# Performance work log

Hardware: AMD Instinct MI355X
Metric: run time of the kernel (lower is better)

Reference implementation:

```python
import jax, jax.numpy as jnp
import numpy as np

MAX_LENGTH = 252
HID = 768
MLP = 770
NLAB = 36


def setup_inputs() -> dict:
    key = jax.random.key(0)
    ks = jax.random.split(key, 7)
    B = 2
    hidden = jax.random.normal(ks[0], (B, MAX_LENGTH + 1, HID), dtype=jnp.float32)
    pred_spans = jnp.sort(jax.random.randint(ks[1], (B, 2), 0, MAX_LENGTH), axis=1)
    span_mask = jax.random.randint(ks[2], (MAX_LENGTH, MAX_LENGTH), 0, 2).astype(jnp.int32)
    W1 = jax.random.normal(ks[3], (MLP, 2 * HID + 1), dtype=jnp.float32) * 0.02
    b1 = jax.random.normal(ks[4], (MLP,), dtype=jnp.float32) * 0.02
    W2 = jax.random.normal(ks[5], (NLAB, MLP), dtype=jnp.float32) * 0.02
    b2 = jax.random.normal(ks[6], (NLAB,), dtype=jnp.float32) * 0.02
    return {"hidden": hidden, "pred_spans": pred_spans, "span_mask": span_mask,
            "W1": W1, "b1": b1, "W2": W2, "b2": b2}


def reference(hidden, pred_spans, span_mask, W1, b1, W2, b2):
    L = MAX_LENGTH
    B = hidden.shape[0]
    vecs = hidden[:, 1:L + 1, :]                      # [B, L, 768] (skip [CLS])
    # Split concat-weight: feat = [vec_i, vec_j, indicator]
    W1i = W1[:, :HID]                                 # [770, 768]
    W1j = W1[:, HID:2 * HID]                          # [770, 768]
    w1c = W1[:, 2 * HID]                              # [770]
    Ai = jnp.einsum('bld,hd->blh', vecs, W1i)         # [B, L, 770]
    Aj = jnp.einsum('bld,hd->blh', vecs, W1j)         # [B, L, 770]
    # Predicate-span indicator: 2 if (i,j)==pred_span; 1 if strictly inside
    # combinations_with_replacement(start..end) minus (start,end); else 0.
    ii = jnp.arange(L)[:, None]
    jj = jnp.arange(L)[None, :]
    s = pred_spans[:, 0][:, None, None]
    e = pred_spans[:, 1][:, None, None]
    eq = (ii == s) & (jj == e)
    inside = (s <= ii) & (ii <= jj) & (jj <= e)
    ind = jnp.where(eq, 2.0, jnp.where(inside, 1.0, 0.0)).astype(hidden.dtype)  # [B,L,L]
    h = Ai[:, :, None, :] + Aj[:, None, :, :] + ind[..., None] * w1c + b1       # [B,L,L,770]
    h = jax.nn.relu(h)
    out = jnp.einsum('bijh,kh->bijk', h, W2) + b2     # [B, L, L, 36]
    valid = (span_mask >= 1)[None, :, :, None]
    out = jnp.where(valid, out, 0.0)                  # invalid pairs -> exact zeros
    out = out.reshape(B, L * L, NLAB)                 # pair dim = 63504
    res = jax.nn.log_softmax(out, axis=1)             # softmax over span pairs
    return jnp.transpose(res, (0, 2, 1))              # [B, 36, L*L]
```

## Files before the change

kernel.cpp:

```cpp
#include <hip/hip_runtime.h>
#include <hip/hip_bf16.h>
#include <math.h>

#define L 252
#define HID 768
#define MLP 770
#define NLAB 36
#define NB 2
#define M1 (NB*L)
#define N1 (2*MLP)
#define LL (L*L)
#define LL4 (LL/4)
#define KC 25
#define KC1 24

typedef float f32x4 __attribute__((ext_vector_type(4)));
typedef short short8 __attribute__((ext_vector_type(8)));

#define AJF_OFF 0
#define AJF_FLOATS 204800
#define AIB_OFF (AJF_OFF + AJF_FLOATS)
#define AIB_FLOATS 604800
#define W2F_OFF (AIB_OFF + AIB_FLOATS)
#define W2F_FLOATS 19200
#define PART_OFF (W2F_OFF + W2F_FLOATS)
#define PART_FLOATS (72*1024*2)

__device__ __forceinline__ void dma16(const void* g, void* l) {
  __builtin_amdgcn_global_load_lds(
      (const __attribute__((address_space(1))) unsigned int*)g,
      (__attribute__((address_space(3))) unsigned int*)l, 16, 0, 0);
}

__device__ __forceinline__ unsigned short bf16b(float x) {
  __hip_bfloat16 h = __float2bfloat16(x);
  return *reinterpret_cast<unsigned short*>(&h);
}

__global__ __launch_bounds__(256) void gemm1_kernel(const float* __restrict__ hid,
                                                    const float* __restrict__ b1,
                                                    const float* __restrict__ W1,
                                                    const float* __restrict__ W2,
                                                    unsigned short* __restrict__ AJF,
                                                    unsigned short* __restrict__ AiBh,
                                                    uint4* __restrict__ W2F) {
  int t = threadIdx.x;
  if (blockIdx.y == 0 && t < 192) {
    int kcw = blockIdx.x;
    int tile = t / 64, lane2 = t - tile * 64;
    int label = tile * 16 + (lane2 & 15);
    int kb = kcw * 32 + (lane2 >> 4) * 8;
    unsigned int u[4];
#pragma unroll
    for (int p = 0; p < 4; p++) {
      unsigned short us[2];
#pragma unroll
      for (int q = 0; q < 2; q++) {
        int k = kb + 2 * p + q;
        float v = (label < NLAB && k < MLP) ? W2[label * MLP + k] : 0.f;
        us[q] = bf16b(v);
      }
      u[p] = (unsigned int)us[0] | ((unsigned int)us[1] << 16);
    }
    W2F[kcw * 192 + t] = make_uint4(u[0], u[1], u[2], u[3]);
  }

  int wave = t >> 6, lane = t & 63, lj = lane & 15, kh = lane >> 4;
  int nt0 = blockIdx.x * 4;
  int m0 = blockIdx.y * 64 + wave * 16;
  int m = m0 + lj;
  int mc = (m < M1) ? m : (M1 - 1);
  int bb = (mc >= L) ? 1 : 0;
  const float* hrow = hid + ((size_t)(bb * (L + 1) + 1 + (mc - bb * L))) * HID + kh * 8;

  const float* rp[4];
#pragma unroll
  for (int nt = 0; nt < 4; nt++) {
    int n = (nt0 + nt) * 16 + lj;
    int nc = (n < N1) ? n : 0;
    rp[nt] = (nc < MLP) ? (W1 + (size_t)nc * 1537)
                        : (W1 + (size_t)(nc - MLP) * 1537 + HID);
  }

  f32x4 acc[4];
#pragma unroll
  for (int nt = 0; nt < 4; nt++) acc[nt] = (f32x4)(0.f);

  union FU { unsigned u[4]; short8 s8; };

  float4 h0 = *(const float4*)(hrow);
  float4 h1 = *(const float4*)(hrow + 4);
  float bw[4][8];
#pragma unroll
  for (int nt = 0; nt < 4; nt++)
#pragma unroll
    for (int e = 0; e < 8; e++) bw[nt][e] = rp[nt][kh * 8 + e];

  for (int kc = 0; kc < KC1; kc++) {
    FU af;
    {
      __hip_bfloat162 p0 = __float22bfloat162_rn(make_float2(h0.x, h0.y));
      __hip_bfloat162 p1 = __float22bfloat162_rn(make_float2(h0.z, h0.w));
      __hip_bfloat162 p2 = __float22bfloat162_rn(make_float2(h1.x, h1.y));
      __hip_bfloat162 p3 = __float22bfloat162_rn(make_float2(h1.z, h1.w));
      af.u[0] = *reinterpret_cast<unsigned*>(&p0);
      af.u[1] = *reinterpret_cast<unsigned*>(&p1);
      af.u[2] = *reinterpret_cast<unsigned*>(&p2);
      af.u[3] = *reinterpret_cast<unsigned*>(&p3);
    }
    FU cb[4];
#pragma unroll
    for (int nt = 0; nt < 4; nt++) {
#pragma unroll
      for (int q = 0; q < 4; q++) {
        __hip_bfloat162 pk = __float22bfloat162_rn(make_float2(bw[nt][2 * q], bw[nt][2 * q + 1]));
        cb[nt].u[q] = *reinterpret_cast<unsigned*>(&pk);
      }
    }
    int kn = kc + 1;
    if (kn < KC1) {
      h0 = *(const float4*)(hrow + kn * 32);
      h1 = *(const float4*)(hrow + kn * 32 + 4);
#pragma unroll
      for (int nt = 0; nt < 4; nt++)
#pragma unroll
        for (int e = 0; e < 8; e++) bw[nt][e] = rp[nt][kn * 32 + kh * 8 + e];
    }
#pragma unroll
    for (int nt = 0; nt < 4; nt++)
      acc[nt] = __builtin_amdgcn_mfma_f32_16x16x32_bf16(af.s8, cb[nt].s8, acc[nt], 0, 0, 0);
  }

#pragma unroll
  for (int nt = 0; nt < 4; nt++) {
    int nn = (nt0 + nt) * 16 + lj;
    if (nn >= N1) continue;
    if (nn < MLP) {
      float b1v = b1[nn];
      float wv = W1[(size_t)nn * 1537 + 1536];
#pragma unroll
      for (int r = 0; r < 4; r++) {
        int mm = m0 + kh * 4 + r;
        if (mm < M1) {
          float a = acc[nt][r] + b1v;
          AiBh[(size_t)(0 * M1 + mm) * 800 + nn] = bf16b(a);
          AiBh[(size_t)(1 * M1 + mm) * 800 + nn] = bf16b(a + wv);
          AiBh[(size_t)(2 * M1 + mm) * 800 + nn] = bf16b(a + 2.f * wv);
        }
      }
    } else {
      int hh = nn - MLP;
      int kcq = hh >> 5, kk = hh & 31;
      int l2hi = (kk >> 3) << 4, ee = kk & 7;
#pragma unroll
      for (int r = 0; r < 4; r++) {
        int mm = m0 + kh * 4 + r;
        if (mm < M1) {
          int bb2 = (mm >= L) ? 1 : 0;
          int jg = mm - bb2 * L;
          size_t rec = ((size_t)((bb2 * KC + kcq) * 16 + (jg >> 4)) * 64 + (l2hi | (jg & 15)));
          AJF[rec * 8 + ee] = bf16b(acc[nt][r]);
        }
      }
    }
  }
}

__global__ __launch_bounds__(256, 2) void main_kernel(
    const unsigned short* __restrict__ AJF,
    const unsigned short* __restrict__ AiBh,
    const uint4* __restrict__ wfr,
    const float* __restrict__ b2,
    const int* __restrict__ spans,
    const int* __restrict__ smask,
    float* __restrict__ out,
    float* __restrict__ part) {
  __shared__ char sm[16384];
  int t = threadIdx.x;
  int wave = t >> 6, lane = t & 63, lj = lane & 15, kh = lane >> 4;
  int j0 = blockIdx.x * 64;
  int i0 = blockIdx.y * 4;
  int b = blockIdx.z;
  int s = spans[2 * b], e = spans[2 * b + 1];
  int j = j0 + wave * 16 + lj;

  int pidx[4];
#pragma unroll
  for (int ii = 0; ii < 4; ii++) {
    int i = i0 + ii;
    int ind = 0;
    if (i == s && j == e) ind = 2;
    else if (s <= i && i <= j && j <= e) ind = 1;
    pidx[ii] = 256 + (ind * 4 + ii) * 4 + kh;
  }

  const unsigned short* aj_g = AJF + ((size_t)((b * KC + 0) * 16 + (j0 >> 4) + wave) * 64 + lane) * 8;
  int pr = lane >> 2; if (pr > 11) pr = 11;
  int pt = pr >> 2, pii = pr & 3, pc = lane & 3;
  const unsigned short* p_g = AiBh + (size_t)(pt * M1 + b * L + i0 + pii) * 800 + pc * 8;
  const uint4* wf_g = wfr + lane;

  f32x4 acc[4][3];
#pragma unroll
  for (int ii = 0; ii < 4; ii++)
#pragma unroll
    for (int tl = 0; tl < 3; tl++) acc[ii][tl] = (f32x4)(0.f);

  union FU { unsigned u[4]; short8 s8; };

  {
    char* bfb = sm;
    dma16(aj_g, bfb + (wave << 10));
    if (wave == 1) dma16(p_g, bfb + 4096);
    if (wave == 0) {
      dma16(&wf_g[0 * 64], bfb + 5120);
      dma16(&wf_g[1 * 64], bfb + 6144);
      dma16(&wf_g[2 * 64], bfb + 7168);
    }
  }

  for (int kc = 0; kc < KC; kc++) {
    __syncthreads();
    int kn = kc + 1;
    if (kn < KC) {
      char* bfb = sm + ((kn & 1) << 13);
      dma16(aj_g + (size_t)kn * 8192, bfb + (wave << 10));
      if (wave == 1) dma16(p_g + kn * 32, bfb + 4096);
      if (wave == 0) {
        dma16(&wf_g[(kn * 3 + 0) * 64], bfb + 5120);
        dma16(&wf_g[(kn * 3 + 1) * 64], bfb + 6144);
        dma16(&wf_g[(kn * 3 + 2) * 64], bfb + 7168);
      }
    }
    const uint4* bu = (const uint4*)(sm + ((kc & 1) << 13));
    uint4 av = bu[(wave << 6) + lane];
    uint4 w0 = bu[320 + lane];
    uint4 w1 = bu[384 + lane];
    uint4 w2v = bu[448 + lane];
    float ajf[8];
    ajf[0] = __uint_as_float(av.x << 16); ajf[1] = __uint_as_float(av.x & 0xFFFF0000u);
    ajf[2] = __uint_as_float(av.y << 16); ajf[3] = __uint_as_float(av.y & 0xFFFF0000u);
    ajf[4] = __uint_as_float(av.z << 16); ajf[5] = __uint_as_float(av.z & 0xFFFF0000u);
    ajf[6] = __uint_as_float(av.w << 16); ajf[7] = __uint_as_float(av.w & 0xFFFF0000u);
    FU wf0, wf1, wf2;
    wf0.u[0] = w0.x; wf0.u[1] = w0.y; wf0.u[2] = w0.z; wf0.u[3] = w0.w;
    wf1.u[0] = w1.x; wf1.u[1] = w1.y; wf1.u[2] = w1.z; wf1.u[3] = w1.w;
    wf2.u[0] = w2v.x; wf2.u[1] = w2v.y; wf2.u[2] = w2v.z; wf2.u[3] = w2v.w;
#pragma unroll
    for (int ii = 0; ii < 4; ii++) {
      uint4 pv = bu[pidx[ii]];
      unsigned pu[4] = {pv.x, pv.y, pv.z, pv.w};
      FU fr;
#pragma unroll
      for (int q = 0; q < 4; q++) {
        float x0 = fmaxf(ajf[2 * q] + __uint_as_float(pu[q] << 16), 0.f);
        float x1 = fmaxf(ajf[2 * q + 1] + __uint_as_float(pu[q] & 0xFFFF0000u), 0.f);
        __hip_bfloat162 pk = __float22bfloat162_rn(make_float2(x0, x1));
        fr.u[q] = *reinterpret_cast<unsigned*>(&pk);
      }
      acc[ii][0] = __builtin_amdgcn_mfma_f32_16x16x32_bf16(fr.s8, wf0.s8, acc[ii][0], 0, 0, 0);
      acc[ii][1] = __builtin_amdgcn_mfma_f32_16x16x32_bf16(fr.s8, wf1.s8, acc[ii][1], 0, 0, 0);
      acc[ii][2] = __builtin_amdgcn_mfma_f32_16x16x32_bf16(fr.s8, wf2.s8, acc[ii][2], 0, 0, 0);
    }
  }

  float v[4][3][4];
#pragma unroll
  for (int ii = 0; ii < 4; ii++) {
    int i = i0 + ii;
    int smv[4];
#pragma unroll
    for (int r = 0; r < 4; r++) {
      int jr = j0 + wave * 16 + kh * 4 + r;
      smv[r] = (jr < L) ? smask[(size_t)i * L + jr] : 0;
    }
#pragma unroll
    for (int tl = 0; tl < 3; tl++) {
      int label = tl * 16 + lj;
      bool lab_ok = label < NLAB;
      float bbv = lab_ok ? b2[label] : 0.f;
#pragma unroll
      for (int r = 0; r < 4; r++) {
        int jr = j0 + wave * 16 + kh * 4 + r;
        float vv = -1e30f;
        if (jr < L && lab_ok) {
          vv = (smv[r] >= 1) ? acc[ii][tl][r] + bbv : 0.f;
          out[(size_t)(b * NLAB + label) * LL + (size_t)i * L + jr] = vv;
        }
        v[ii][tl][r] = vv;
      }
    }
  }
#pragma unroll
  for (int tl = 0; tl < 3; tl++) {
    float mx = -1e30f;
#pragma unroll
    for (int ii = 0; ii < 4; ii++)
#pragma unroll
      for (int r = 0; r < 4; r++) mx = fmaxf(mx, v[ii][tl][r]);
    mx = fmaxf(mx, __shfl_xor(mx, 16, 64));
    mx = fmaxf(mx, __shfl_xor(mx, 32, 64));
    float ssum = 0.f;
#pragma unroll
    for (int ii = 0; ii < 4; ii++)
#pragma unroll
      for (int r = 0; r < 4; r++) {
        float vv = v[ii][tl][r];
        ssum += (vv > -1e29f) ? __expf(vv - mx) : 0.f;
      }
    ssum += __shfl_xor(ssum, 16, 64);
    ssum += __shfl_xor(ssum, 32, 64);
    int label = tl * 16 + lj;
    if (kh == 0 && label < NLAB) {
      int slot = (blockIdx.x * 63 + blockIdx.y) * 4 + wave;
      float2* pp = (float2*)part + (size_t)(b * NLAB + label) * 1024 + slot;
      *pp = make_float2(mx, ssum);
    }
  }
}

__global__ __launch_bounds__(256) void finish_kernel(const float* __restrict__ part,
                                                     float* __restrict__ out) {
  int bk = blockIdx.y, cx = blockIdx.x;
  int t = threadIdx.x, wave = t >> 6, lane = t & 63;
  const float2* pp = (const float2*)part + (size_t)bk * 1024;
  float m = -1e30f, ss = 0.f;
  for (int idx = t; idx < 1008; idx += 256) {
    float2 q = pp[idx];
    if (q.x > m) { ss = ss * __expf(m - q.x) + q.y; m = q.x; }
    else ss += q.y * __expf(q.x - m);
  }
#pragma unroll
  for (int o = 1; o < 64; o <<= 1) {
    float m2 = __shfl_xor(m, o, 64);
    float s2 = __shfl_xor(ss, o, 64);
    if (m2 > m) { ss = ss * __expf(m - m2) + s2; m = m2; }
    else ss += s2 * __expf(m2 - m);
  }
  __shared__ float rm[4], rs[4], lsh;
  if (lane == 0) { rm[wave] = m; rs[wave] = ss; }
  __syncthreads();
  if (t == 0) {
    float M = rm[0], S = rs[0];
#pragma unroll
    for (int w = 1; w < 4; w++) {
      float m2 = rm[w], s2 = rs[w];
      if (m2 > M) { S = S * __expf(M - m2) + s2; M = m2; }
      else S += s2 * __expf(m2 - M);
    }
    lsh = M + logf(S);
  }
  __syncthreads();
  float l = lsh;
  float4* po = (float4*)(out + (size_t)bk * LL);
  int start = cx * 1985;
  int end = start + 1985; if (end > LL4) end = LL4;
  for (int idx = start + t; idx < end; idx += 256) {
    float4 v = po[idx];
    v.x -= l; v.y -= l; v.z -= l; v.w -= l;
    po[idx] = v;
  }
}

extern "C" void kernel_launch(void* const* d_in, const int* in_sizes, int n_in,
                              void* d_out, int out_size, void* d_ws, size_t ws_size,
                              hipStream_t stream) {
  const float* hidden = (const float*)d_in[0];
  const int* spans    = (const int*)d_in[1];
  const int* smask    = (const int*)d_in[2];
  const float* W1     = (const float*)d_in[3];
  const float* b1     = (const float*)d_in[4];
  const float* W2     = (const float*)d_in[5];
  const float* b2     = (const float*)d_in[6];
  float* ws = (float*)d_ws;
  unsigned short* AJF  = (unsigned short*)(ws + AJF_OFF);
  unsigned short* AiBh = (unsigned short*)(ws + AIB_OFF);
  uint4* W2F           = (uint4*)(ws + W2F_OFF);
  float* part          = ws + PART_OFF;
  float* out = (float*)d_out;

  gemm1_kernel<<<dim3(25, 8), 256, 0, stream>>>(hidden, b1, W1, W2, AJF, AiBh, W2F);
  main_kernel<<<dim3(4, 63, NB), 256, 0, stream>>>(AJF, AiBh, (const uint4*)W2F, b2,
                                                   spans, smask, out, part);
  finish_kernel<<<dim3(8, NB * NLAB), 256, 0, stream>>>(part, out);
}
```

Before: 155.8 us.

## Prepack bf16 operands and use per-wave LDS DMA pipelines without block barriers

Adds a pack kernel that converts W1, W2 and the hidden rows to bf16 MFMA fragment layout ahead of time. gemm1 then streams these fragments through per-wave double-buffered LDS via global_load_lds instead of doing strided fp32 loads and converting inline. main_kernel drops __syncthreads: each wave loads its own copy of the P and W2 fragments into a private LDS region and waits only on its own vmcnt. This costs an extra launch, redundant per-wave loads, and more LDS per block (40 KB), which may lower occupancy.

```diff
diff --git a/kernel.cpp b/kernel.cpp
--- a/kernel.cpp
+++ b/kernel.cpp
@@ -13,6 +13,8 @@
 #define LL4 (LL/4)
 #define KC 25
 #define KC1 24
+#define NT1P 100
+#define NMT 32
 
 typedef float f32x4 __attribute__((ext_vector_type(4)));
 typedef short short8 __attribute__((ext_vector_type(8)));
@@ -25,6 +27,13 @@
 #define W2F_FLOATS 19200
 #define PART_OFF (W2F_OFF + W2F_FLOATS)
 #define PART_FLOATS (72*1024*2)
+#define W1F_OFF (PART_OFF + PART_FLOATS)
+#define W1F_FLOATS (KC1*NT1P*64*4)
+#define VBF_OFF (W1F_OFF + W1F_FLOATS)
+#define VBF_FLOATS (NMT*KC1*64*4)
+#define NW1F (KC1*NT1P*64)
+#define NW2F (KC*3*64)
+#define NVBF (NMT*KC1*64)
 
 __device__ __forceinline__ void dma16(const void* g, void* l) {
   __builtin_amdgcn_global_load_lds(
@@ -37,19 +46,42 @@
   return *reinterpret_cast<unsigned short*>(&h);
 }
 
-__global__ __launch_bounds__(256) void gemm1_kernel(const float* __restrict__ hid,
-                                                    const float* __restrict__ b1,
-                                                    const float* __restrict__ W1,
-                                                    const float* __restrict__ W2,
-                                                    unsigned short* __restrict__ AJF,
-                                                    unsigned short* __restrict__ AiBh,
-                                                    uint4* __restrict__ W2F) {
-  int t = threadIdx.x;
-  if (blockIdx.y == 0 && t < 192) {
-    int kcw = blockIdx.x;
-    int tile = t / 64, lane2 = t - tile * 64;
-    int label = tile * 16 + (lane2 & 15);
-    int kb = kcw * 32 + (lane2 >> 4) * 8;
+#define WAIT_VM0() __builtin_amdgcn_s_waitcnt(0x0F70)
+
+__global__ __launch_bounds__(256) void pack_kernel(const float* __restrict__ W1,
+                                                   const float* __restrict__ W2,
+                                                   const float* __restrict__ hid,
+                                                   float* __restrict__ ws) {
+  const int total = NW1F + NW2F + NVBF;
+  int idx = blockIdx.x * 256 + threadIdx.x;
+  if (idx >= total) return;
+  if (idx < NW1F) {
+    int kc = idx / (NT1P * 64);
+    int rem = idx - kc * (NT1P * 64);
+    int nt = rem / 64, lane = rem - nt * 64;
+    int n = nt * 16 + (lane & 15);
+    int kb = kc * 32 + (lane >> 4) * 8;
+    unsigned int u[4];
+#pragma unroll
+    for (int p = 0; p < 4; p++) {
+      unsigned short us[2];
+#pragma unroll
+      for (int q = 0; q < 2; q++) {
+        int k = kb + 2 * p + q;
+        float v = 0.f;
+        if (n < N1) v = (n < MLP) ? W1[(size_t)n * 1537 + k]
+                                  : W1[(size_t)(n - MLP) * 1537 + HID + k];
+        us[q] = bf16b(v);
+      }
+      u[p] = (unsigned int)us[0] | ((unsigned int)us[1] << 16);
+    }
+    ((uint4*)(ws + W1F_OFF))[idx] = make_uint4(u[0], u[1], u[2], u[3]);
+  } else if (idx < NW1F + NW2F) {
+    int e2 = idx - NW1F;
+    int kc = e2 / 192, rem = e2 - kc * 192;
+    int tile = rem / 64, lane = rem - tile * 64;
+    int label = tile * 16 + (lane & 15);
+    int kb = kc * 32 + (lane >> 4) * 8;
     unsigned int u[4];
 #pragma unroll
     for (int p = 0; p < 4; p++) {
@@ -62,73 +94,77 @@
       }
       u[p] = (unsigned int)us[0] | ((unsigned int)us[1] << 16);
     }
-    W2F[kcw * 192 + t] = make_uint4(u[0], u[1], u[2], u[3]);
-  }
-
+    ((uint4*)(ws + W2F_OFF))[e2] = make_uint4(u[0], u[1], u[2], u[3]);
+  } else {
+    int e3 = idx - NW1F - NW2F;
+    int mt = e3 / (KC1 * 64);
+    int rem = e3 - mt * (KC1 * 64);
+    int kc = rem / 64, lane = rem - kc * 64;
+    int m = mt * 16 + (lane & 15);
+    int kb = kc * 32 + (lane >> 4) * 8;
+    unsigned int u[4] = {0u, 0u, 0u, 0u};
+    if (m < M1) {
+      int b = (m >= L) ? 1 : 0;
+      const float* src = hid + ((size_t)(b * (L + 1) + 1 + (m - b * L))) * HID + kb;
+      float4 v0 = *(const float4*)src;
+      float4 v1 = *(const float4*)(src + 4);
+      float vv[8] = {v0.x, v0.y, v0.z, v0.w, v1.x, v1.y, v1.z, v1.w};
+#pragma unroll
+      for (int p = 0; p < 4; p++)
+        u[p] = (unsigned int)bf16b(vv[2 * p]) | ((unsigned int)bf16b(vv[2 * p + 1]) << 16);
+    }
+    ((uint4*)(ws + VBF_OFF))[e3] = make_uint4(u[0], u[1], u[2], u[3]);
+  }
+}
+
+__global__ __launch_bounds__(256, 2) void gemm1_kernel(const float* __restrict__ b1,
+                                                       const float* __restrict__ W1,
+                                                       const float* __restrict__ ws_ro,
+                                                       unsigned short* __restrict__ AJF,
+                                                       unsigned short* __restrict__ AiBh) {
+  __shared__ char sm[40960];
+  int t = threadIdx.x;
   int wave = t >> 6, lane = t & 63, lj = lane & 15, kh = lane >> 4;
   int nt0 = blockIdx.x * 4;
-  int m0 = blockIdx.y * 64 + wave * 16;
-  int m = m0 + lj;
-  int mc = (m < M1) ? m : (M1 - 1);
-  int bb = (mc >= L) ? 1 : 0;
-  const float* hrow = hid + ((size_t)(bb * (L + 1) + 1 + (mc - bb * L))) * HID + kh * 8;
-
-  const float* rp[4];
-#pragma unroll
-  for (int nt = 0; nt < 4; nt++) {
-    int n = (nt0 + nt) * 16 + lj;
-    int nc = (n < N1) ? n : 0;
-    rp[nt] = (nc < MLP) ? (W1 + (size_t)nc * 1537)
-                        : (W1 + (size_t)(nc - MLP) * 1537 + HID);
-  }
+  int mt = blockIdx.y * 4 + wave;
+  int m0 = mt * 16;
+  const uint4* vbf = (const uint4*)(ws_ro + VBF_OFF) + (size_t)mt * KC1 * 64 + lane;
+  const uint4* w1f = (const uint4*)(ws_ro + W1F_OFF);
+  char* WB = sm + wave * 10240;
 
   f32x4 acc[4];
 #pragma unroll
   for (int nt = 0; nt < 4; nt++) acc[nt] = (f32x4)(0.f);
-
   union FU { unsigned u[4]; short8 s8; };
 
-  float4 h0 = *(const float4*)(hrow);
-  float4 h1 = *(const float4*)(hrow + 4);
-  float bw[4][8];
-#pragma unroll
-  for (int nt = 0; nt < 4; nt++)
-#pragma unroll
-    for (int e = 0; e < 8; e++) bw[nt][e] = rp[nt][kh * 8 + e];
+  dma16(vbf, WB);
+#pragma unroll
+  for (int q = 0; q < 4; q++)
+    dma16(&w1f[(size_t)(0 * NT1P + nt0 + q) * 64 + lane], WB + 1024 + q * 1024);
 
   for (int kc = 0; kc < KC1; kc++) {
-    FU af;
-    {
-      __hip_bfloat162 p0 = __float22bfloat162_rn(make_float2(h0.x, h0.y));
-      __hip_bfloat162 p1 = __float22bfloat162_rn(make_float2(h0.z, h0.w));
-      __hip_bfloat162 p2 = __float22bfloat162_rn(make_float2(h1.x, h1.y));
-      __hip_bfloat162 p3 = __float22bfloat162_rn(make_float2(h1.z, h1.w));
-      af.u[0] = *reinterpret_cast<unsigned*>(&p0);
-      af.u[1] = *reinterpret_cast<unsigned*>(&p1);
-      af.u[2] = *reinterpret_cast<unsigned*>(&p2);
-      af.u[3] = *reinterpret_cast<unsigned*>(&p3);
-    }
-    FU cb[4];
-#pragma unroll
-    for (int nt = 0; nt < 4; nt++) {
-#pragma unroll
-      for (int q = 0; q < 4; q++) {
-        __hip_bfloat162 pk = __float22bfloat162_rn(make_float2(bw[nt][2 * q], bw[nt][2 * q + 1]));
-        cb[nt].u[q] = *reinterpret_cast<unsigned*>(&pk);
-      }
-    }
+    WAIT_VM0();
+    const char* bufc = WB + ((kc & 1) * 5120);
+    uint4 av = *(const uint4*)(bufc + lane * 16);
+    uint4 bv[4];
+#pragma unroll
+    for (int q = 0; q < 4; q++) bv[q] = *(const uint4*)(bufc + 1024 + q * 1024 + lane * 16);
+    __builtin_amdgcn_sched_barrier(0);
     int kn = kc + 1;
     if (kn < KC1) {
-      h0 = *(const float4*)(hrow + kn * 32);
-      h1 = *(const float4*)(hrow + kn * 32 + 4);
-#pragma unroll
-      for (int nt = 0; nt < 4; nt++)
-#pragma unroll
-        for (int e = 0; e < 8; e++) bw[nt][e] = rp[nt][kn * 32 + kh * 8 + e];
-    }
-#pragma unroll
-    for (int nt = 0; nt < 4; nt++)
-      acc[nt] = __builtin_amdgcn_mfma_f32_16x16x32_bf16(af.s8, cb[nt].s8, acc[nt], 0, 0, 0);
+      char* bufn = WB + ((kn & 1) * 5120);
+      dma16(vbf + kn * 64, bufn);
+#pragma unroll
+      for (int q = 0; q < 4; q++)
+        dma16(&w1f[(size_t)(kn * NT1P + nt0 + q) * 64 + lane], bufn + 1024 + q * 1024);
+    }
+    __builtin_amdgcn_sched_barrier(0);
+    FU af; af.u[0] = av.x; af.u[1] = av.y; af.u[2] = av.z; af.u[3] = av.w;
+#pragma unroll
+    for (int q = 0; q < 4; q++) {
+      FU bf; bf.u[0] = bv[q].x; bf.u[1] = bv[q].y; bf.u[2] = bv[q].z; bf.u[3] = bv[q].w;
+      acc[q] = __builtin_amdgcn_mfma_f32_16x16x32_bf16(af.s8, bf.s8, acc[q], 0, 0, 0);
+    }
   }
 
 #pragma unroll
@@ -175,7 +211,7 @@
     const int* __restrict__ smask,
     float* __restrict__ out,
     float* __restrict__ part) {
-  __shared__ char sm[16384];
+  __shared__ char sm[40960];
   int t = threadIdx.x;
   int wave = t >> 6, lane = t & 63, lj = lane & 15, kh = lane >> 4;
   int j0 = blockIdx.x * 64;
@@ -184,14 +220,14 @@
   int s = spans[2 * b], e = spans[2 * b + 1];
   int j = j0 + wave * 16 + lj;
 
-  int pidx[4];
+  int poff[4];
 #pragma unroll
   for (int ii = 0; ii < 4; ii++) {
     int i = i0 + ii;
     int ind = 0;
     if (i == s && j == e) ind = 2;
     else if (s <= i && i <= j && j <= e) ind = 1;
-    pidx[ii] = 256 + (ind * 4 + ii) * 4 + kh;
+    poff[ii] = 1024 + ((ind * 4 + ii) * 4 + kh) * 16;
   }
 
   const unsigned short* aj_g = AJF + ((size_t)((b * KC + 0) * 16 + (j0 >> 4) + wave) * 64 + lane) * 8;
@@ -199,44 +235,42 @@
   int pt = pr >> 2, pii = pr & 3, pc = lane & 3;
   const unsigned short* p_g = AiBh + (size_t)(pt * M1 + b * L + i0 + pii) * 800 + pc * 8;
   const uint4* wf_g = wfr + lane;
+  char* WB = sm + wave * 10240;
 
   f32x4 acc[4][3];
 #pragma unroll
   for (int ii = 0; ii < 4; ii++)
 #pragma unroll
     for (int tl = 0; tl < 3; tl++) acc[ii][tl] = (f32x4)(0.f);
-
   union FU { unsigned u[4]; short8 s8; };
 
-  {
-    char* bfb = sm;
-    dma16(aj_g, bfb + (wave << 10));
-    if (wave == 1) dma16(p_g, bfb + 4096);
-    if (wave == 0) {
-      dma16(&wf_g[0 * 64], bfb + 5120);
-      dma16(&wf_g[1 * 64], bfb + 6144);
-      dma16(&wf_g[2 * 64], bfb + 7168);
-    }
-  }
+  dma16(aj_g, WB);
+  dma16(p_g, WB + 1024);
+  dma16(&wf_g[0 * 64], WB + 2048);
+  dma16(&wf_g[1 * 64], WB + 3072);
+  dma16(&wf_g[2 * 64], WB + 4096);
 
   for (int kc = 0; kc < KC; kc++) {
-    __syncthreads();
+    WAIT_VM0();
+    const char* bufc = WB + ((kc & 1) * 5120);
+    uint4 av = *(const uint4*)(bufc + lane * 16);
+    uint4 w0 = *(const uint4*)(bufc + 2048 + lane * 16);
+    uint4 w1 = *(const uint4*)(bufc + 3072 + lane * 16);
+    uint4 w2v = *(const uint4*)(bufc + 4096 + lane * 16);
+    uint4 pv[4];
+#pragma unroll
+    for (int ii = 0; ii < 4; ii++) pv[ii] = *(const uint4*)(bufc + poff[ii]);
+    __builtin_amdgcn_sched_barrier(0);
     int kn = kc + 1;
     if (kn < KC) {
-      char* bfb = sm + ((kn & 1) << 13);
-      dma16(aj_g + (size_t)kn * 8192, bfb + (wave << 10));
-      if (wave == 1) dma16(p_g + kn * 32, bfb + 4096);
-      if (wave == 0) {
-        dma16(&wf_g[(kn * 3 + 0) * 64], bfb + 5120);
-        dma16(&wf_g[(kn * 3 + 1) * 64], bfb + 6144);
-        dma16(&wf_g[(kn * 3 + 2) * 64], bfb + 7168);
-      }
-    }
-    const uint4* bu = (const uint4*)(sm + ((kc & 1) << 13));
-    uint4 av = bu[(wave << 6) + lane];
-    uint4 w0 = bu[320 + lane];
-    uint4 w1 = bu[384 + lane];
-    uint4 w2v = bu[448 + lane];
+      char* bufn = WB + ((kn & 1) * 5120);
+      dma16(aj_g + (size_t)kn * 8192, bufn);
+      dma16(p_g + kn * 32, bufn + 1024);
+      dma16(&wf_g[(kn * 3 + 0) * 64], bufn + 2048);
+      dma16(&wf_g[(kn * 3 + 1) * 64], bufn + 3072);
+      dma16(&wf_g[(kn * 3 + 2) * 64], bufn + 4096);
+    }
+    __builtin_amdgcn_sched_barrier(0);
     float ajf[8];
     ajf[0] = __uint_as_float(av.x << 16); ajf[1] = __uint_as_float(av.x & 0xFFFF0000u);
     ajf[2] = __uint_as_float(av.y << 16); ajf[3] = __uint_as_float(av.y & 0xFFFF0000u);
@@ -248,8 +282,7 @@
     wf2.u[0] = w2v.x; wf2.u[1] = w2v.y; wf2.u[2] = w2v.z; wf2.u[3] = w2v.w;
 #pragma unroll
     for (int ii = 0; ii < 4; ii++) {
-      uint4 pv = bu[pidx[ii]];
-      unsigned pu[4] = {pv.x, pv.y, pv.z, pv.w};
+      unsigned pu[4] = {pv[ii].x, pv[ii].y, pv[ii].z, pv[ii].w};
       FU fr;
 #pragma unroll
       for (int q = 0; q < 4; q++) {
@@ -375,12 +408,13 @@
   float* ws = (float*)d_ws;
   unsigned short* AJF  = (unsigned short*)(ws + AJF_OFF);
   unsigned short* AiBh = (unsigned short*)(ws + AIB_OFF);
-  uint4* W2F           = (uint4*)(ws + W2F_OFF);
+  const uint4* wfr     = (const uint4*)(ws + W2F_OFF);
   float* part          = ws + PART_OFF;
   float* out = (float*)d_out;
 
-  gemm1_kernel<<<dim3(25, 8), 256, 0, stream>>>(hidden, b1, W1, W2, AJF, AiBh, W2F);
-  main_kernel<<<dim3(4, 63, NB), 256, 0, stream>>>(AJF, AiBh, (const uint4*)W2F, b2,
-                                                   spans, smask, out, part);
+  const int total_pack = NW1F + NW2F + NVBF;
+  pack_kernel<<<(total_pack + 255) / 256, 256, 0, stream>>>(W1, W2, hidden, ws);
+  gemm1_kernel<<<dim3(25, 8), 256, 0, stream>>>(b1, W1, ws, AJF, AiBh);
+  main_kernel<<<dim3(4, 63, NB), 256, 0, stream>>>(AJF, AiBh, wfr, b2, spans, smask, out, part);
   finish_kernel<<<dim3(8, NB * NLAB), 256, 0, stream>>>(part, out);
 }
```

After: 138.2 us. -11.3%, faster.
